# Performance work log

Hardware: AMD Instinct MI355X
Metric: run time of the kernel (lower is better)

Reference implementation:

```python
import jax, jax.numpy as jnp
import numpy as np

B = 8192
I_SIZE = 1024
H_SIZE = 1024
C2 = 2.7183  # module's hard-coded e approximation

def setup_inputs() -> dict:
    key = jax.random.key(0)
    k0, k1, k2, k3, k4 = jax.random.split(key, 5)
    input_tensor = jax.random.uniform(k0, (B, I_SIZE + 1), dtype=jnp.float32)  # last col = dt >= 0
    h_cur = jax.random.normal(k1, (B, H_SIZE), dtype=jnp.float32)
    c_cur = jax.random.normal(k2, (B, H_SIZE), dtype=jnp.float32)
    W_layers = jax.random.normal(k3, (4 * H_SIZE, I_SIZE + H_SIZE), dtype=jnp.float32) * 0.02
    b_layers = jnp.zeros((4 * H_SIZE,), dtype=jnp.float32)
    W_desc = jax.random.normal(k4, (H_SIZE, H_SIZE), dtype=jnp.float32) * 0.02
    b_desc = jnp.zeros((H_SIZE,), dtype=jnp.float32)
    return {"input_tensor": input_tensor, "h_cur": h_cur, "c_cur": c_cur,
            "W_layers": W_layers, "b_layers": b_layers,
            "W_desc": W_desc, "b_desc": b_desc}

def reference(input_tensor, h_cur, c_cur, W_layers, b_layers, W_desc, b_desc):
    x = input_tensor[:, :-1]          # [B, I]
    dt = input_tensor[:, -1:]         # [B, 1]
    # map_elapse_time: T = 1/log(t + e), broadcast over h_size (matmul with ones == broadcast)
    T = 1.0 / jnp.log(dt + C2)        # [B, 1]
    C_ST = jnp.tanh(h_cur @ W_desc.T + b_desc)          # [B, H]
    h_adj = h_cur - C_ST + T * C_ST                     # decayed short-term memory
    combined = jnp.concatenate([x, h_adj], axis=1)      # [B, I+H]
    gates = combined @ W_layers.T + b_layers            # [B, 4H]
    cc_i, cc_f, cc_o, cc_g = jnp.split(gates, 4, axis=1)
    i = jax.nn.sigmoid(cc_i)
    f = jax.nn.sigmoid(cc_f)
    o = jax.nn.sigmoid(cc_o)
    g = jnp.tanh(cc_g)
    c_next = f * c_cur + i * g
    h_next = o * jnp.tanh(c_next)
    return (h_next, c_next)
```

## Files before the change

### kernel.cpp

```cpp
#include <hip/hip_runtime.h>
#include <hip/hip_bf16.h>
#include <math.h>

typedef __bf16 bf16x8 __attribute__((ext_vector_type(8)));
typedef float  f32x4  __attribute__((ext_vector_type(4)));

#define B_ROWS 8192
#define HSZ    1024

#define GLOAD16(gsrc, ldst)                                                          \
  __builtin_amdgcn_global_load_lds((const __attribute__((address_space(1))) void*)(gsrc), \
                                   (__attribute__((address_space(3))) void*)(ldst),  \
                                   16, 0, 0)

__device__ inline unsigned short f2bf(float f) {
  union { float f; unsigned u; } x; x.f = f;
  unsigned r = x.u + 0x7fffu + ((x.u >> 16) & 1u);
  return (unsigned short)(r >> 16);
}

__device__ inline float sigm(float x) { return 1.0f / (1.0f + __expf(-x)); }

__global__ void k_convert(const float* __restrict__ inp,
                          const float* __restrict__ h,
                          const float* __restrict__ Wl,
                          const float* __restrict__ Wd,
                          unsigned short* __restrict__ comb,
                          unsigned short* __restrict__ Wlb,
                          unsigned short* __restrict__ hb,
                          unsigned short* __restrict__ Wdb,
                          float* __restrict__ Tm1) {
  const long stride = (long)gridDim.x * blockDim.x;
  const long tid0 = (long)blockIdx.x * blockDim.x + threadIdx.x;

#define CNV8(dst, s0, s1) { ushort4 u0, u1;                                   \
    u0.x = f2bf(s0.x); u0.y = f2bf(s0.y); u0.z = f2bf(s0.z); u0.w = f2bf(s0.w); \
    u1.x = f2bf(s1.x); u1.y = f2bf(s1.y); u1.z = f2bf(s1.z); u1.w = f2bf(s1.w); \
    *(ushort4*)(dst) = u0; *(ushort4*)((dst) + 4) = u1; }

  for (long i = tid0; i < (long)B_ROWS * HSZ / 8; i += stride) {
    float4 v0 = ((const float4*)h)[i * 2], v1 = ((const float4*)h)[i * 2 + 1];
    CNV8(hb + i * 8, v0, v1);
  }
  for (long i = tid0; i < (long)B_ROWS * HSZ / 8; i += stride) {
    long e = i * 8; long b = e >> 10; long c = e & 1023;
    const float* s = inp + b * 1025 + c;
    float4 v0 = *(const float4*)s, v1 = *(const float4*)(s + 4);
    CNV8(comb + b * 2048 + c, v0, v1);
  }
  for (long i = tid0; i < 4096L * 2048 / 8; i += stride) {
    float4 v0 = ((const float4*)Wl)[i * 2], v1 = ((const float4*)Wl)[i * 2 + 1];
    CNV8(Wlb + i * 8, v0, v1);
  }
  for (long i = tid0; i < 1024L * 1024 / 8; i += stride) {
    float4 v0 = ((const float4*)Wd)[i * 2], v1 = ((const float4*)Wd)[i * 2 + 1];
    CNV8(Wdb + i * 8, v0, v1);
  }
  for (long i = tid0; i < B_ROWS; i += stride) {
    float dt = inp[i * 1025 + 1024];
    Tm1[i] = 1.0f / logf(dt + 2.7183f) - 1.0f;
  }
#undef CNV8
}

__global__ void k_gemm1(const unsigned short* __restrict__ A,
                        const unsigned short* __restrict__ Bm,
                        const float* __restrict__ h,
                        const float* __restrict__ bd,
                        const float* __restrict__ Tm1,
                        unsigned short* __restrict__ comb) {
  const int K = 1024;
  __shared__ __align__(16) unsigned short As[128 * 32];
  __shared__ __align__(16) unsigned short Bs[128 * 32];
  const int tid = threadIdx.x;
  const int lane = tid & 63;
  const int wave = tid >> 6;
  const int wr = wave >> 1, wc = wave & 1;
  const int bRow = blockIdx.x;
  const int bCol = blockIdx.y;

  const int sRow = tid >> 2;
  const int sK = (tid & 3) * 8;
  const unsigned short* aSrc0 = A + (long)(bRow * 128 + sRow) * K + sK;
  const unsigned short* aSrc1 = A + (long)(bRow * 128 + 64 + sRow) * K + sK;
  const unsigned short* bSrc0 = Bm + (long)(bCol * 128 + sRow) * K + sK;
  const unsigned short* bSrc1 = Bm + (long)(bCol * 128 + 64 + sRow) * K + sK;
  unsigned short* aDst0 = As + tid * 8;
  unsigned short* aDst1 = As + 2048 + tid * 8;
  unsigned short* bDst0 = Bs + tid * 8;
  unsigned short* bDst1 = Bs + 2048 + tid * 8;

  f32x4 acc[4][4] = {};
  const int fr = lane & 15, fk = (lane >> 4) * 8;

  for (int k0 = 0; k0 < K; k0 += 32) {
    GLOAD16(aSrc0 + k0, aDst0);
    GLOAD16(aSrc1 + k0, aDst1);
    GLOAD16(bSrc0 + k0, bDst0);
    GLOAD16(bSrc1 + k0, bDst1);
    __syncthreads();
    bf16x8 a[4], b[4];
#pragma unroll
    for (int m = 0; m < 4; m++) a[m] = *(const bf16x8*)(As + (wr * 64 + m * 16 + fr) * 32 + fk);
#pragma unroll
    for (int n = 0; n < 4; n++) b[n] = *(const bf16x8*)(Bs + (wc * 64 + n * 16 + fr) * 32 + fk);
#pragma unroll
    for (int m = 0; m < 4; m++)
#pragma unroll
      for (int n = 0; n < 4; n++)
        acc[m][n] = __builtin_amdgcn_mfma_f32_16x16x32_bf16(a[m], b[n], acc[m][n], 0, 0, 0);
    __syncthreads();
  }

  const int cr = (lane >> 4) * 4;
  const int cc = lane & 15;
#pragma unroll
  for (int m = 0; m < 4; m++)
#pragma unroll
    for (int n = 0; n < 4; n++) {
      const int col = bCol * 128 + wc * 64 + n * 16 + cc;
#pragma unroll
      for (int r = 0; r < 4; r++) {
        const int row = bRow * 128 + wr * 64 + m * 16 + cr + r;
        float v = acc[m][n][r] + bd[col];
        float cst = tanhf(v);
        float hadj = h[(long)row * HSZ + col] + Tm1[row] * cst;
        comb[(long)row * 2048 + 1024 + col] = f2bf(hadj);
      }
    }
}

#define NT2 64
__global__ __launch_bounds__(512, 2)
void k_gemm2_np(const unsigned short* __restrict__ A,
                const unsigned short* __restrict__ Bm,
                const float* __restrict__ bl,
                const float* __restrict__ c_cur,
                float* __restrict__ out) {
  __shared__ __align__(16) unsigned short lds[4][16384];

  const int tid = threadIdx.x;
  const int lane = tid & 63;
  const int wid = tid >> 6;
  const int wr = wid >> 2;
  const int wc = wid & 3;

  const int bid = blockIdx.x;
  const int xcd = bid & 7;
  const int ii = bid >> 3;
  const int sweep = ii >> 5;
  const int pos = ii & 31;
  const int bRow = xcd * 4 + sweep * 2 + (pos & 1);
  const int bCol = pos >> 1;

  const int sr = tid >> 2;
  const int swsel = (sr >> 1) & 3;
  const int gk = ((tid & 3) ^ swsel) << 3;
  const unsigned short* aBase = A + (long)(bRow * 256 + sr) * 2048 + gk;
  const int rl0 = sr, rl1 = 128 + sr;
  const int grow0 = ((rl0 >> 4) & 3) * 1024 + bCol * 64 + (rl0 >> 6) * 16 + (rl0 & 15);
  const int grow1 = ((rl1 >> 4) & 3) * 1024 + bCol * 64 + (rl1 >> 6) * 16 + (rl1 & 15);
  const unsigned short* bBase0 = Bm + (long)grow0 * 2048 + gk;
  const unsigned short* bBase1 = Bm + (long)grow1 * 2048 + gk;

#define STAGE_A2(slot, tt) { unsigned short* d_ = &lds[slot][0] + tid * 8;        \
    GLOAD16(aBase + (long)(tt) * 32, d_);                                          \
    GLOAD16(aBase + 128L * 2048 + (long)(tt) * 32, d_ + 512 * 8); }
#define STAGE_B2(slot, tt) { unsigned short* d_ = &lds[slot][8192] + tid * 8;     \
    GLOAD16(bBase0 + (long)(tt) * 32, d_);                                         \
    GLOAD16(bBase1 + (long)(tt) * 32, d_ + 512 * 8); }

  const int fr = lane & 15, q = lane >> 4;
  int offA[8], offB[4];
#pragma unroll
  for (int m = 0; m < 8; m++) {
    const int row = wr * 128 + m * 16 + fr;
    offA[m] = row * 32 + ((q ^ ((row >> 1) & 3)) << 3);
  }
#pragma unroll
  for (int n = 0; n < 4; n++) {
    const int row = wc * 64 + n * 16 + fr;
    offB[n] = 8192 + row * 32 + ((q ^ ((row >> 1) & 3)) << 3);
  }

  f32x4 acc[8][4] = {};
  bf16x8 aC[8], bC[4], aN[8], bN[4];

  STAGE_A2(0, 0); STAGE_B2(0, 0);
  STAGE_A2(1, 1); STAGE_B2(1, 1);
  STAGE_A2(2, 2); STAGE_B2(2, 2);
  asm volatile("s_waitcnt vmcnt(8)" ::: "memory");
  __builtin_amdgcn_s_barrier();
#pragma unroll
  for (int n = 0; n < 4; n++) bC[n] = *(const bf16x8*)(&lds[0][0] + offB[n]);
#pragma unroll
  for (int m = 0; m < 8; m++) aC[m] = *(const bf16x8*)(&lds[0][0] + offA[m]);

#define TILE(t, aCur, bCur, aNxt, bNxt, VM, DOREAD, DOSTAGE)                         \
  {                                                                                  \
    asm volatile("s_waitcnt vmcnt(" #VM ")" ::: "memory");                           \
    __builtin_amdgcn_s_barrier();                                                    \
    if (DOREAD) {                                                                    \
      const unsigned short* bufN = &lds[((t) + 1) & 3][0];                           \
      _Pragma("unroll")                                                              \
      for (int n = 0; n < 4; n++) bNxt[n] = *(const bf16x8*)(bufN + offB[n]);        \
      _Pragma("unroll")                                                              \
      for (int m = 0; m < 8; m++) aNxt[m] = *(const bf16x8*)(bufN + offA[m]);        \
    }                                                                                \
    if (DOSTAGE) { STAGE_A2(((t) + 3) & 3, (t) + 3); STAGE_B2(((t) + 3) & 3, (t) + 3); } \
    _Pragma("unroll")                                                                \
    for (int m = 0; m < 8; m++)                                                      \
      _Pragma("unroll")                                                              \
      for (int n = 0; n < 4; n++)                                                    \
        acc[m][n] = __builtin_amdgcn_mfma_f32_16x16x32_bf16(aCur[m], bCur[n], acc[m][n], 0, 0, 0); \
  }

  for (int t = 0; t < 60; t += 2) {
    TILE(t,     aC, bC, aN, bN, 4, true, true);
    TILE(t + 1, aN, bN, aC, bC, 4, true, true);
  }
  TILE(60, aC, bC, aN, bN, 4, true,  true);
  TILE(61, aN, bN, aC, bC, 4, true,  false);
  TILE(62, aC, bC, aN, bN, 0, true,  false);
  TILE(63, aN, bN, aC, bC, 0, false, false);
#undef TILE

  const int cr = (lane >> 4) * 4;
  const int cc = lane & 15;
  const int j = bCol * 64 + wc * 16 + cc;
#pragma unroll
  for (int m = 0; m < 8; m++) {
#pragma unroll
    for (int r = 0; r < 4; r++) {
      const int row = bRow * 256 + wr * 128 + m * 16 + cr + r;
      float iv = sigm(acc[m][0][r] + bl[j]);
      float fv = sigm(acc[m][1][r] + bl[1024 + j]);
      float ov = sigm(acc[m][2][r] + bl[2048 + j]);
      float gv = tanhf(acc[m][3][r] + bl[3072 + j]);
      float cn = fv * c_cur[(long)row * HSZ + j] + iv * gv;
      float hn = ov * tanhf(cn);
      out[(long)row * HSZ + j] = hn;
      out[(long)B_ROWS * HSZ + (long)row * HSZ + j] = cn;
    }
  }
}

extern "C" void kernel_launch(void* const* d_in, const int* in_sizes, int n_in,
                              void* d_out, int out_size, void* d_ws, size_t ws_size,
                              hipStream_t stream) {
  const float* inp = (const float*)d_in[0];
  const float* h   = (const float*)d_in[1];
  const float* c   = (const float*)d_in[2];
  const float* Wl  = (const float*)d_in[3];
  const float* bl  = (const float*)d_in[4];
  const float* Wd  = (const float*)d_in[5];
  const float* bd  = (const float*)d_in[6];

  char* ws = (char*)d_ws;
  unsigned short* comb = (unsigned short*)(ws);
  unsigned short* Wlb  = (unsigned short*)(ws + 33554432);
  unsigned short* hb   = (unsigned short*)(ws + 50331648);
  unsigned short* Wdb  = (unsigned short*)(ws + 67108864);
  float*          Tm1  = (float*)(ws + 69206016);
  float*          out  = (float*)d_out;

  hipLaunchKernelGGL(k_convert, dim3(2048), dim3(256), 0, stream,
                     inp, h, Wl, Wd, comb, Wlb, hb, Wdb, Tm1);
  hipLaunchKernelGGL(k_gemm1, dim3(64, 8), dim3(256), 0, stream,
                     hb, Wdb, h, bd, Tm1, comb);
  hipLaunchKernelGGL(k_gemm2_np, dim3(512), dim3(512), 0, stream,
                     comb, Wlb, bl, c, out);
}
```

Baseline: 226.1 us.

## Warp-specialize gate GEMM with dedicated producer waves for global-to-LDS loads

Adds four producer waves per block that only stream A and B tiles from global memory into the four-slot LDS ring. The eight compute waves now just read LDS fragments, issue MFMAs and hit barriers, with no global load issue or vmcnt waits of their own. The goal is to move load-issue overhead off the MFMA waves and overlap it more fully with compute. In exchange the block grows to 768 threads with launch bounds of 3 blocks per CU. That can tighten the register budget and cause spills of the large accumulator set, and since LDS use stays at 128KB per block it does not raise occupancy.

```diff
diff --git a/kernel.cpp b/kernel.cpp
--- a/kernel.cpp
+++ b/kernel.cpp
@@ -131,8 +131,8 @@
 }
 
 #define NT2 64
-__global__ __launch_bounds__(512, 2)
-void k_gemm2_np(const unsigned short* __restrict__ A,
+__global__ __launch_bounds__(768, 3)
+void k_gemm2_ws(const unsigned short* __restrict__ A,
                 const unsigned short* __restrict__ Bm,
                 const float* __restrict__ bl,
                 const float* __restrict__ c_cur,
@@ -142,8 +142,6 @@
   const int tid = threadIdx.x;
   const int lane = tid & 63;
   const int wid = tid >> 6;
-  const int wr = wid >> 2;
-  const int wc = wid & 3;
 
   const int bid = blockIdx.x;
   const int xcd = bid & 7;
@@ -153,23 +151,49 @@
   const int bRow = xcd * 4 + sweep * 2 + (pos & 1);
   const int bCol = pos >> 1;
 
-  const int sr = tid >> 2;
-  const int swsel = (sr >> 1) & 3;
-  const int gk = ((tid & 3) ^ swsel) << 3;
-  const unsigned short* aBase = A + (long)(bRow * 256 + sr) * 2048 + gk;
-  const int rl0 = sr, rl1 = 128 + sr;
-  const int grow0 = ((rl0 >> 4) & 3) * 1024 + bCol * 64 + (rl0 >> 6) * 16 + (rl0 & 15);
-  const int grow1 = ((rl1 >> 4) & 3) * 1024 + bCol * 64 + (rl1 >> 6) * 16 + (rl1 & 15);
-  const unsigned short* bBase0 = Bm + (long)grow0 * 2048 + gk;
-  const unsigned short* bBase1 = Bm + (long)grow1 * 2048 + gk;
-
-#define STAGE_A2(slot, tt) { unsigned short* d_ = &lds[slot][0] + tid * 8;        \
-    GLOAD16(aBase + (long)(tt) * 32, d_);                                          \
-    GLOAD16(aBase + 128L * 2048 + (long)(tt) * 32, d_ + 512 * 8); }
-#define STAGE_B2(slot, tt) { unsigned short* d_ = &lds[slot][8192] + tid * 8;     \
-    GLOAD16(bBase0 + (long)(tt) * 32, d_);                                         \
-    GLOAD16(bBase1 + (long)(tt) * 32, d_ + 512 * 8); }
-
+  if (wid >= 8) {
+    const int t2 = tid - 512;
+    const int sr = t2 >> 2;
+    const int swsel = (sr >> 1) & 3;
+    const int gk = ((t2 & 3) ^ swsel) << 3;
+    const unsigned short* aS0 = A + (long)(bRow * 256 +   0 + sr) * 2048 + gk;
+    const unsigned short* aS1 = A + (long)(bRow * 256 +  64 + sr) * 2048 + gk;
+    const unsigned short* aS2 = A + (long)(bRow * 256 + 128 + sr) * 2048 + gk;
+    const unsigned short* aS3 = A + (long)(bRow * 256 + 192 + sr) * 2048 + gk;
+#define GROWF(rl) ((((rl) >> 4) & 3) * 1024 + bCol * 64 + ((rl) >> 6) * 16 + ((rl) & 15))
+    const unsigned short* bS0 = Bm + (long)GROWF(0   + sr) * 2048 + gk;
+    const unsigned short* bS1 = Bm + (long)GROWF(64  + sr) * 2048 + gk;
+    const unsigned short* bS2 = Bm + (long)GROWF(128 + sr) * 2048 + gk;
+    const unsigned short* bS3 = Bm + (long)GROWF(192 + sr) * 2048 + gk;
+#undef GROWF
+#define STG(slot, tt) { unsigned short* d_ = &lds[slot][0] + t2 * 8;       \
+    GLOAD16(aS0 + (long)(tt) * 32, d_);                                     \
+    GLOAD16(aS1 + (long)(tt) * 32, d_ + 2048);                              \
+    GLOAD16(aS2 + (long)(tt) * 32, d_ + 4096);                              \
+    GLOAD16(aS3 + (long)(tt) * 32, d_ + 6144);                              \
+    GLOAD16(bS0 + (long)(tt) * 32, d_ + 8192);                              \
+    GLOAD16(bS1 + (long)(tt) * 32, d_ + 10240);                             \
+    GLOAD16(bS2 + (long)(tt) * 32, d_ + 12288);                             \
+    GLOAD16(bS3 + (long)(tt) * 32, d_ + 14336); }
+
+    STG(0, 0); STG(1, 1); STG(2, 2);
+    asm volatile("s_waitcnt vmcnt(8)" ::: "memory");
+    __builtin_amdgcn_s_barrier();
+    for (int t = 0; t < NT2; ++t) {
+      if (t <= 60) {
+        STG((t + 3) & 3, t + 3);
+        asm volatile("s_waitcnt vmcnt(8)" ::: "memory");
+      } else if (t == 61) {
+        asm volatile("s_waitcnt vmcnt(0)" ::: "memory");
+      }
+      __builtin_amdgcn_s_barrier();
+    }
+#undef STG
+    return;
+  }
+
+  const int wr = wid >> 2;
+  const int wc = wid & 3;
   const int fr = lane & 15, q = lane >> 4;
   int offA[8], offB[4];
 #pragma unroll
@@ -186,44 +210,34 @@
   f32x4 acc[8][4] = {};
   bf16x8 aC[8], bC[4], aN[8], bN[4];
 
-  STAGE_A2(0, 0); STAGE_B2(0, 0);
-  STAGE_A2(1, 1); STAGE_B2(1, 1);
-  STAGE_A2(2, 2); STAGE_B2(2, 2);
-  asm volatile("s_waitcnt vmcnt(8)" ::: "memory");
   __builtin_amdgcn_s_barrier();
 #pragma unroll
   for (int n = 0; n < 4; n++) bC[n] = *(const bf16x8*)(&lds[0][0] + offB[n]);
 #pragma unroll
   for (int m = 0; m < 8; m++) aC[m] = *(const bf16x8*)(&lds[0][0] + offA[m]);
 
-#define TILE(t, aCur, bCur, aNxt, bNxt, VM, DOREAD, DOSTAGE)                         \
-  {                                                                                  \
-    asm volatile("s_waitcnt vmcnt(" #VM ")" ::: "memory");                           \
-    __builtin_amdgcn_s_barrier();                                                    \
-    if (DOREAD) {                                                                    \
-      const unsigned short* bufN = &lds[((t) + 1) & 3][0];                           \
-      _Pragma("unroll")                                                              \
-      for (int n = 0; n < 4; n++) bNxt[n] = *(const bf16x8*)(bufN + offB[n]);        \
-      _Pragma("unroll")                                                              \
-      for (int m = 0; m < 8; m++) aNxt[m] = *(const bf16x8*)(bufN + offA[m]);        \
-    }                                                                                \
-    if (DOSTAGE) { STAGE_A2(((t) + 3) & 3, (t) + 3); STAGE_B2(((t) + 3) & 3, (t) + 3); } \
+#define MF(aSet, bSet)                                                               \
     _Pragma("unroll")                                                                \
     for (int m = 0; m < 8; m++)                                                      \
       _Pragma("unroll")                                                              \
       for (int n = 0; n < 4; n++)                                                    \
-        acc[m][n] = __builtin_amdgcn_mfma_f32_16x16x32_bf16(aCur[m], bCur[n], acc[m][n], 0, 0, 0); \
-  }
-
-  for (int t = 0; t < 60; t += 2) {
-    TILE(t,     aC, bC, aN, bN, 4, true, true);
-    TILE(t + 1, aN, bN, aC, bC, 4, true, true);
-  }
-  TILE(60, aC, bC, aN, bN, 4, true,  true);
-  TILE(61, aN, bN, aC, bC, 4, true,  false);
-  TILE(62, aC, bC, aN, bN, 0, true,  false);
-  TILE(63, aN, bN, aC, bC, 0, false, false);
-#undef TILE
+        acc[m][n] = __builtin_amdgcn_mfma_f32_16x16x32_bf16(aSet[m], bSet[n], acc[m][n], 0, 0, 0);
+#define RD(aSet, bSet, slotptr)                                                      \
+    _Pragma("unroll")                                                                \
+    for (int n = 0; n < 4; n++) bSet[n] = *(const bf16x8*)((slotptr) + offB[n]);     \
+    _Pragma("unroll")                                                                \
+    for (int m = 0; m < 8; m++) aSet[m] = *(const bf16x8*)((slotptr) + offA[m]);
+
+  for (int t = 0; t < NT2; t += 2) {
+    if (t < NT2 - 1) { RD(aN, bN, &lds[(t + 1) & 3][0]); }
+    MF(aC, bC);
+    __builtin_amdgcn_s_barrier();
+    if (t + 2 < NT2) { RD(aC, bC, &lds[(t + 2) & 3][0]); }
+    MF(aN, bN);
+    __builtin_amdgcn_s_barrier();
+  }
+#undef MF
+#undef RD
 
   const int cr = (lane >> 4) * 4;
   const int cc = lane & 15;
@@ -268,6 +282,6 @@
                      inp, h, Wl, Wd, comb, Wlb, hb, Wdb, Tm1);
   hipLaunchKernelGGL(k_gemm1, dim3(64, 8), dim3(256), 0, stream,
                      hb, Wdb, h, bd, Tm1, comb);
-  hipLaunchKernelGGL(k_gemm2_np, dim3(512), dim3(512), 0, stream,
+  hipLaunchKernelGGL(k_gemm2_ws, dim3(512), dim3(768), 0, stream,
                      comb, Wlb, bl, c, out);
 }
```

Measured after the change: 862.2 us. 281% more time.
